# Kernel optimization log

Measured on AMD Instinct MI355X. Metric: run time of the kernel, lower is better.

The kernel has to match this reference:

```python
import jax, jax.numpy as jnp
import numpy as np

# Static configuration (matches init_kwargs)
B, D, H, W, C = 8, 4, 64, 64, 256
WS = (4, 8, 8)            # (temporal, h, w) window size
HEADS = 8
HD = C // HEADS
HID = 512                 # MLP hidden
N = WS[0] * WS[1] * WS[2]          # tokens per window = 256
INTERVAL = WS[1] * WS[2]           # tokens per frame in a window = 64
BW = B * (D // WS[0]) * (H // WS[1]) * (W // WS[2])  # total windows = 512
RPB_SIZE = (2 * WS[0] - 1) * (2 * WS[1] - 1) * (2 * WS[2] - 1)  # 1575


def _rel_index(ws):
    """Standard Swin-3D relative position index table, shape (N, N)."""
    d, h, w = ws
    coords = np.stack(np.meshgrid(np.arange(d), np.arange(h), np.arange(w), indexing='ij'))
    cf = coords.reshape(3, -1)
    rel = (cf[:, :, None] - cf[:, None, :]).transpose(1, 2, 0)
    rel[..., 0] += d - 1
    rel[..., 1] += h - 1
    rel[..., 2] += w - 1
    rel[..., 0] *= (2 * h - 1) * (2 * w - 1)
    rel[..., 1] *= (2 * w - 1)
    return rel.sum(-1)


_REL = _rel_index(WS)
# Per temporal group i: queries = frame i tokens, keys = all OTHER tokens (complement)
_KEY_IDS_NP = [np.array([j for j in range(N) if not (i * INTERVAL <= j < (i + 1) * INTERVAL)])
               for i in range(WS[0])]
KEY_IDS = [jnp.asarray(k) for k in _KEY_IDS_NP]
BIAS_IDX = [jnp.asarray(_REL[i * INTERVAL:(i + 1) * INTERVAL][:, _KEY_IDS_NP[i]])
            for i in range(WS[0])]


def setup_inputs() -> dict:
    key = jax.random.key(0)
    ks = jax.random.split(key, 8)
    s = jnp.float32(0.02)
    return {
        'x': jax.random.normal(ks[0], (B, D, H, W, C), jnp.float32),
        'ln1_g': jnp.ones((C,), jnp.float32), 'ln1_b': jnp.zeros((C,), jnp.float32),
        'ln2_g': jnp.ones((C,), jnp.float32), 'ln2_b': jnp.zeros((C,), jnp.float32),
        'wq': jax.random.normal(ks[1], (C, C), jnp.float32) * s,
        'wkv': jax.random.normal(ks[2], (C, 2 * C), jnp.float32) * s,
        'wp': jax.random.normal(ks[3], (C, C), jnp.float32) * s,
        'bp': jnp.zeros((C,), jnp.float32),
        'rpb': jax.random.normal(ks[4], (RPB_SIZE, HEADS), jnp.float32) * s,
        'w1': jax.random.normal(ks[5], (C, HID), jnp.float32) * s,
        'b1': jnp.zeros((HID,), jnp.float32),
        'w2': jax.random.normal(ks[6], (HID, C), jnp.float32) * s,
        'b2': jnp.zeros((C,), jnp.float32),
    }


def _ln(x, g, b):
    m = x.mean(-1, keepdims=True)
    v = ((x - m) ** 2).mean(-1, keepdims=True)
    return (x - m) * jax.lax.rsqrt(v + 1e-5) * g + b


def _partition(x):  # (B,D,H,W,C) -> (BW, N, C)
    x = x.reshape(B, D // WS[0], WS[0], H // WS[1], WS[1], W // WS[2], WS[2], C)
    return x.transpose(0, 1, 3, 5, 2, 4, 6, 7).reshape(BW, N, C)


def _reverse(xw):  # (BW, N, C) -> (B,D,H,W,C)
    x = xw.reshape(B, D // WS[0], H // WS[1], W // WS[2], WS[0], WS[1], WS[2], C)
    return x.transpose(0, 1, 4, 2, 5, 3, 6, 7).reshape(B, D, H, W, C)


def _window_attn(xw, wq, wkv, wp, bp, rpb):
    # q/k/v: (BW, heads, N, HD)
    q = (xw @ wq).reshape(BW, N, HEADS, HD).transpose(0, 2, 1, 3)
    kv = (xw @ wkv).reshape(BW, N, 2, HEADS, HD).transpose(2, 0, 3, 1, 4)
    k, v = kv[0], kv[1]
    scale = jnp.float32(HD ** -0.5)
    outs = []
    for i in range(WS[0]):  # loop over temporal groups (static, small)
        qs = q[:, :, i * INTERVAL:(i + 1) * INTERVAL] * scale   # (BW,h,Nq,HD)
        ks = k[:, :, KEY_IDS[i]]                                 # (BW,h,Nk,HD)
        vs = v[:, :, KEY_IDS[i]]
        bias = rpb[BIAS_IDX[i]].transpose(2, 0, 1)               # (h,Nq,Nk)
        a = jnp.einsum('bhqd,bhkd->bhqk', qs, ks) + bias[None]
        a = jax.nn.softmax(a, axis=-1)
        o = jnp.einsum('bhqk,bhkd->bhqd', a, vs)
        outs.append(o.transpose(0, 2, 1, 3).reshape(BW, INTERVAL, C))
    return jnp.concatenate(outs, axis=1) @ wp + bp


def reference(x, ln1_g, ln1_b, ln2_g, ln2_b, wq, wkv, wp, bp, rpb, w1, b1, w2, b2):
    xw = _partition(_ln(x, ln1_g, ln1_b))
    x = x + _reverse(_window_attn(xw, wq, wkv, wp, bp, rpb))
    h = jax.nn.gelu(_ln(x, ln2_g, ln2_b) @ w1 + b1, approximate=False)
    return x + h @ w2 + b2
```

## Files before the change

kernel.cpp:

```cpp
#include <hip/hip_runtime.h>

typedef unsigned short u16;
typedef __bf16 bf16x8 __attribute__((ext_vector_type(8)));
typedef float floatx4 __attribute__((ext_vector_type(4)));
typedef unsigned short u16x8 __attribute__((ext_vector_type(8)));

#define C_  256
#define NTOK 131072
#define QSCALE 0.17677669529663687f
#define RPB_N 1575

#define R1_ELEMS 33554432ull

__device__ u16 g_wT[524288];

__device__ __forceinline__ float bf2f(u16 u) {
    return __uint_as_float(((unsigned)u) << 16);
}
__device__ __forceinline__ u16 f2bf(float f) {
    unsigned u = __float_as_uint(f);
    return (u16)((u + 0x7FFFu + ((u >> 16) & 1u)) >> 16);
}

#define GL16(gsrc, ldst) __builtin_amdgcn_global_load_lds(                    \
    (const __attribute__((address_space(1))) void*)(gsrc),                    \
    (__attribute__((address_space(3))) void*)(ldst), 16, 0, 0)

__global__ __launch_bounds__(256) void wcvt_kernel(
    const float* __restrict__ W, int N, int ks, int ofs)
{
    const int idx = blockIdx.x * 256 + threadIdx.x;
    const int n = idx >> ks;
    const int k = idx & ((1 << ks) - 1);
    g_wT[ofs + idx] = f2bf(W[(size_t)k * N + n]);
}

__global__ __launch_bounds__(256) void ln_part_kernel(
    const float* __restrict__ x, const float* __restrict__ g, const float* __restrict__ bb,
    u16* __restrict__ xw)
{
    const int lane = threadIdx.x & 63;
    const int wave = threadIdx.x >> 6;
    const int t = blockIdx.x * 4 + wave;
    const int wb = t >> 8, n = t & 255;
    const int bidx = wb >> 6, hb = (wb >> 3) & 7, wbl = wb & 7;
    const int d = n >> 6, hh = (n >> 3) & 7, ww = n & 7;
    const size_t src = ((((size_t)bidx * 4 + d) * 64 + hb * 8 + hh) * 64 + wbl * 8 + ww) * C_;
    const int c0 = lane * 4;
    float4 raw = *reinterpret_cast<const float4*>(&x[src + c0]);
    float v0 = raw.x, v1 = raw.y, v2 = raw.z, v3 = raw.w;
    float s = v0 + v1 + v2 + v3;
    float sq = v0 * v0 + v1 * v1 + v2 * v2 + v3 * v3;
#pragma unroll
    for (int off = 32; off > 0; off >>= 1) {
        s  += __shfl_xor(s, off, 64);
        sq += __shfl_xor(sq, off, 64);
    }
    const float mean = s * (1.0f / 256.0f);
    const float var  = sq * (1.0f / 256.0f) - mean * mean;
    const float rstd = rsqrtf(var + 1e-5f);
    float4 gr = *reinterpret_cast<const float4*>(&g[c0]);
    float4 br = *reinterpret_cast<const float4*>(&bb[c0]);
    ushort4 outv;
    outv.x = f2bf((v0 - mean) * rstd * gr.x + br.x);
    outv.y = f2bf((v1 - mean) * rstd * gr.y + br.y);
    outv.z = f2bf((v2 - mean) * rstd * gr.z + br.z);
    outv.w = f2bf((v3 - mean) * rstd * gr.w + br.w);
    *reinterpret_cast<ushort4*>(&xw[(size_t)t * C_ + c0]) = outv;
}

__global__ __launch_bounds__(256) void resid_ln2_kernel(
    const float* __restrict__ x, const u16* __restrict__ oproj,
    const float* __restrict__ g, const float* __restrict__ bb,
    float* __restrict__ y, u16* __restrict__ xn)
{
    const int lane = threadIdx.x & 63;
    const int wave = threadIdx.x >> 6;
    const int t = blockIdx.x * 4 + wave;
    const int wpos = t & 63;
    const int h = (t >> 6) & 63;
    const int d = (t >> 12) & 3;
    const int bidx = t >> 14;
    const int wr = (((bidx * 8) + (h >> 3)) * 8 + (wpos >> 3)) * 256
                 + d * 64 + (h & 7) * 8 + (wpos & 7);
    const int c0 = lane * 4;
    float4 xr = *reinterpret_cast<const float4*>(&x[(size_t)t * C_ + c0]);
    ushort4 pr = *reinterpret_cast<const ushort4*>(&oproj[(size_t)wr * C_ + c0]);
    float v0 = xr.x + bf2f(pr.x);
    float v1 = xr.y + bf2f(pr.y);
    float v2 = xr.z + bf2f(pr.z);
    float v3 = xr.w + bf2f(pr.w);
    float s = v0 + v1 + v2 + v3;
    float sq = v0 * v0 + v1 * v1 + v2 * v2 + v3 * v3;
#pragma unroll
    for (int off = 32; off > 0; off >>= 1) {
        s  += __shfl_xor(s, off, 64);
        sq += __shfl_xor(sq, off, 64);
    }
    const float mean = s * (1.0f / 256.0f);
    const float var  = sq * (1.0f / 256.0f) - mean * mean;
    const float rstd = rsqrtf(var + 1e-5f);
    float4 yv; yv.x = v0; yv.y = v1; yv.z = v2; yv.w = v3;
    *reinterpret_cast<float4*>(&y[(size_t)t * C_ + c0]) = yv;
    float4 gr = *reinterpret_cast<const float4*>(&g[c0]);
    float4 br = *reinterpret_cast<const float4*>(&bb[c0]);
    ushort4 nv;
    nv.x = f2bf((v0 - mean) * rstd * gr.x + br.x);
    nv.y = f2bf((v1 - mean) * rstd * gr.y + br.y);
    nv.z = f2bf((v2 - mean) * rstd * gr.z + br.z);
    nv.w = f2bf((v3 - mean) * rstd * gr.w + br.w);
    *reinterpret_cast<ushort4*>(&xn[(size_t)t * C_ + c0]) = nv;
}

__global__ __launch_bounds__(256, 3) void gemm_v3_kernel(
    const u16* __restrict__ A, const u16* __restrict__ A2,
    int bofs, int kdim,
    u16* __restrict__ Cm, float* __restrict__ Cf, const float* __restrict__ bias,
    int mode)
{
    __shared__ __align__(16) u16 lds[2 * 10240];
    const int tid  = threadIdx.x;
    const int lane = tid & 63, wave = tid >> 6;
    const int lr = lane & 15, lq = lane >> 4;
    const int row0 = blockIdx.x * 64;
    const u16* Bt = &g_wT[bofs];

    const int s_row = lane >> 2;
    const int s_kel = (lane & 3) * 8;

    floatx4 acc[4][4] = {};
    const int NK = kdim >> 5;
    int cur = 0;

    auto STAGE = [&](int buf, int ks) {
        const int k0 = ks << 5;
        const u16* Asrc = A;
        int ka = k0;
        if (k0 >= 256) { Asrc = A2; ka = k0 - 256; }
        u16* lb = &lds[buf * 10240];
        GL16(&Asrc[(size_t)(row0 + wave * 16 + s_row) * 256 + ka + s_kel],
             lb + wave * 512 + lane * 8);
#pragma unroll
        for (int c = 0; c < 4; ++c) {
            const int s = wave * 4 + c;
            GL16(&Bt[(size_t)(s * 16 + s_row) * kdim + k0 + s_kel],
                 lb + 2048 + s * 512 + lane * 8);
        }
    };

    STAGE(0, 0);
    __syncthreads();

    for (int ks = 0; ks < NK; ++ks) {
        if (ks + 1 < NK) STAGE(cur ^ 1, ks + 1);
        const u16* lb = &lds[cur * 10240];
        bf16x8 af[4], bfv[4];
#pragma unroll
        for (int mt = 0; mt < 4; ++mt)
            af[mt] = *reinterpret_cast<const bf16x8*>(lb + (mt * 16 + lr) * 32 + lq * 8);
#pragma unroll
        for (int nt = 0; nt < 4; ++nt)
            bfv[nt] = *reinterpret_cast<const bf16x8*>(
                lb + 2048 + (wave * 64 + nt * 16 + lr) * 32 + lq * 8);
#pragma unroll
        for (int mt = 0; mt < 4; ++mt)
#pragma unroll
            for (int nt = 0; nt < 4; ++nt)
                acc[mt][nt] = __builtin_amdgcn_mfma_f32_16x16x32_bf16(
                    af[mt], bfv[nt], acc[mt][nt], 0, 0, 0);
        __syncthreads();
        cur ^= 1;
    }

    float* tw = reinterpret_cast<float*>(&lds[0]) + wave * (16 * 68);
#pragma unroll
    for (int mt = 0; mt < 4; ++mt) {
        asm volatile("s_waitcnt lgkmcnt(0)" ::: "memory");
        __builtin_amdgcn_sched_barrier(0);
#pragma unroll
        for (int nt = 0; nt < 4; ++nt) {
            const int col = wave * 64 + nt * 16 + lr;
            const float bs = (mode != 0) ? bias[col] : 0.0f;
#pragma unroll
            for (int r = 0; r < 4; ++r) {
                float v = acc[mt][nt][r] + bs;
                if (mode == 2) v = 0.5f * v * (1.0f + erff(v * 0.70710678118654752f));
                tw[(lq * 4 + r) * 68 + nt * 16 + lr] = v;
            }
        }
        asm volatile("s_waitcnt lgkmcnt(0)" ::: "memory");
        __builtin_amdgcn_sched_barrier(0);
        const int rrow = lane >> 2, grp = lane & 3;
        const float* src = &tw[rrow * 68 + grp * 16];
        float4 f0 = *reinterpret_cast<const float4*>(src + 0);
        float4 f1 = *reinterpret_cast<const float4*>(src + 4);
        float4 f2 = *reinterpret_cast<const float4*>(src + 8);
        float4 f3 = *reinterpret_cast<const float4*>(src + 12);
        const size_t gofs = (size_t)(row0 + mt * 16 + rrow) * 256 + wave * 64 + grp * 16;
        if (mode == 5) {
            float4* cp = reinterpret_cast<float4*>(&Cf[gofs]);
            float4 c0 = cp[0], c1 = cp[1], c2 = cp[2], c3 = cp[3];
            c0.x += f0.x; c0.y += f0.y; c0.z += f0.z; c0.w += f0.w;
            c1.x += f1.x; c1.y += f1.y; c1.z += f1.z; c1.w += f1.w;
            c2.x += f2.x; c2.y += f2.y; c2.z += f2.z; c2.w += f2.w;
            c3.x += f3.x; c3.y += f3.y; c3.z += f3.z; c3.w += f3.w;
            cp[0] = c0; cp[1] = c1; cp[2] = c2; cp[3] = c3;
        } else {
            const float tf[16] = {f0.x, f0.y, f0.z, f0.w, f1.x, f1.y, f1.z, f1.w,
                                  f2.x, f2.y, f2.z, f2.w, f3.x, f3.y, f3.z, f3.w};
            u16x8 o0, o1;
#pragma unroll
            for (int j = 0; j < 8; ++j) { o0[j] = f2bf(tf[j]); o1[j] = f2bf(tf[j + 8]); }
            *reinterpret_cast<u16x8*>(&Cm[gofs])     = o0;
            *reinterpret_cast<u16x8*>(&Cm[gofs + 8]) = o1;
        }
    }
}

__global__ __launch_bounds__(256) void attn_kernel(
    u16* __restrict__ qo, const u16* __restrict__ kb, const u16* __restrict__ vb,
    const float* __restrict__ rpbp)
{
    __shared__ __align__(16) u16 qh[64][40];
    __shared__ __align__(16) u16 kt[192][40];
    __shared__ __align__(16) u16 vtt[32][200];
    __shared__ __align__(16) u16 sp[64][200];
    __shared__ float biasld[RPB_N + 1];

    const int wb = blockIdx.x >> 2;
    const int i  = blockIdx.x & 3;
    const int tid = threadIdx.x;
    const int lane = tid & 63, wave = tid >> 6;
    const int lr = lane & 15, lq = lane >> 4;
    const size_t qbase = ((size_t)(wb * 256 + i * 64)) * C_;

    int relb[12][4];
    {
        const int q0 = wave * 16 + lq * 4;
#pragma unroll
        for (int r = 0; r < 4; ++r) {
            const int q = q0 + r;
            const int hq = q >> 3, wq_ = q & 7;
#pragma unroll
            for (int t = 0; t < 12; ++t) {
                const int kl = t * 16 + lr;
                const int nk = (kl < i * 64) ? kl : kl + 64;
                const int dk = nk >> 6, hk = (nk >> 3) & 7, wk = nk & 7;
                relb[t][r] = (i - dk + 3) * 225 + (hq - hk + 7) * 15 + (wq_ - wk + 7);
            }
        }
    }

    for (int h = 0; h < 8; ++h) {
        {
            const int row = tid >> 2, g = tid & 3;
            *reinterpret_cast<float4*>(&qh[row][g * 8]) =
                *reinterpret_cast<const float4*>(&qo[qbase + (size_t)row * C_ + h * 32 + g * 8]);
        }
#pragma unroll
        for (int t = 0; t < 3; ++t) {
            const int c = tid + t * 256;
            const int kl = c >> 2, g = c & 3;
            const int nk = (kl < i * 64) ? kl : kl + 64;
            const size_t base = ((size_t)(wb * 256 + nk)) * C_ + h * 32 + g * 8;
            *reinterpret_cast<float4*>(&kt[kl][g * 8]) =
                *reinterpret_cast<const float4*>(&kb[base]);
            u16x8 vv = *reinterpret_cast<const u16x8*>(&vb[base]);
#pragma unroll
            for (int j = 0; j < 8; ++j) vtt[g * 8 + j][kl] = vv[j];
        }
        for (int j = tid; j < RPB_N; j += 256) biasld[j] = rpbp[j * 8 + h];
        __syncthreads();

        floatx4 acc[12];
#pragma unroll
        for (int t = 0; t < 12; ++t) acc[t] = (floatx4){0.f, 0.f, 0.f, 0.f};
        {
            const bf16x8 af = *reinterpret_cast<const bf16x8*>(&qh[wave * 16 + lr][lq * 8]);
#pragma unroll
            for (int t = 0; t < 12; ++t) {
                const bf16x8 bfv = *reinterpret_cast<const bf16x8*>(&kt[t * 16 + lr][lq * 8]);
                acc[t] = __builtin_amdgcn_mfma_f32_16x16x32_bf16(af, bfv, acc[t], 0, 0, 0);
            }
        }

        float mrow[4] = {-1e30f, -1e30f, -1e30f, -1e30f};
#pragma unroll
        for (int t = 0; t < 12; ++t)
#pragma unroll
            for (int r = 0; r < 4; ++r) {
                const float v = fmaf(acc[t][r], QSCALE, biasld[relb[t][r]]);
                acc[t][r] = v;
                mrow[r] = fmaxf(mrow[r], v);
            }
#pragma unroll
        for (int off = 8; off >= 1; off >>= 1)
#pragma unroll
            for (int r = 0; r < 4; ++r)
                mrow[r] = fmaxf(mrow[r], __shfl_xor(mrow[r], off, 64));

        float srow[4] = {0.f, 0.f, 0.f, 0.f};
#pragma unroll
        for (int t = 0; t < 12; ++t)
#pragma unroll
            for (int r = 0; r < 4; ++r) {
                const float e = __expf(acc[t][r] - mrow[r]);
                acc[t][r] = e;
                srow[r] += e;
            }
#pragma unroll
        for (int off = 8; off >= 1; off >>= 1)
#pragma unroll
            for (int r = 0; r < 4; ++r)
                srow[r] += __shfl_xor(srow[r], off, 64);
#pragma unroll
        for (int r = 0; r < 4; ++r) srow[r] = 1.0f / srow[r];

#pragma unroll
        for (int t = 0; t < 12; ++t)
#pragma unroll
            for (int r = 0; r < 4; ++r)
                sp[wave * 16 + lq * 4 + r][t * 16 + lr] = f2bf(acc[t][r] * srow[r]);
        __syncthreads();

        floatx4 oacc[2];
        oacc[0] = (floatx4){0.f, 0.f, 0.f, 0.f};
        oacc[1] = (floatx4){0.f, 0.f, 0.f, 0.f};
#pragma unroll
        for (int kc = 0; kc < 6; ++kc) {
            const bf16x8 pa = *reinterpret_cast<const bf16x8*>(&sp[wave * 16 + lr][kc * 32 + lq * 8]);
#pragma unroll
            for (int nt = 0; nt < 2; ++nt) {
                const bf16x8 bv = *reinterpret_cast<const bf16x8*>(&vtt[nt * 16 + lr][kc * 32 + lq * 8]);
                oacc[nt] = __builtin_amdgcn_mfma_f32_16x16x32_bf16(pa, bv, oacc[nt], 0, 0, 0);
            }
        }
#pragma unroll
        for (int nt = 0; nt < 2; ++nt)
#pragma unroll
            for (int r = 0; r < 4; ++r)
                qo[qbase + (size_t)(wave * 16 + lq * 4 + r) * C_ + h * 32 + nt * 16 + lr] =
                    f2bf(oacc[nt][r]);
        __syncthreads();
    }
}

extern "C" void kernel_launch(void* const* d_in, const int* in_sizes, int n_in,
                              void* d_out, int out_size, void* d_ws, size_t ws_size,
                              hipStream_t stream) {
    const float* x    = (const float*)d_in[0];
    const float* ln1g = (const float*)d_in[1];
    const float* ln1b = (const float*)d_in[2];
    const float* ln2g = (const float*)d_in[3];
    const float* ln2b = (const float*)d_in[4];
    const float* wq   = (const float*)d_in[5];
    const float* wkv  = (const float*)d_in[6];
    const float* wp   = (const float*)d_in[7];
    const float* bp   = (const float*)d_in[8];
    const float* rpb  = (const float*)d_in[9];
    const float* w1   = (const float*)d_in[10];
    const float* b1   = (const float*)d_in[11];
    const float* w2   = (const float*)d_in[12];
    const float* b2   = (const float*)d_in[13];
    float* outf = (float*)d_out;
    u16*   outu = (u16*)d_out;
    u16*   ws16 = (u16*)d_ws;

    u16* r0 = ws16;
    u16* r1 = ws16 + R1_ELEMS;
    u16* kbuf = outu;
    u16* vbuf = outu + R1_ELEMS;

    wcvt_kernel<<<256, 256, 0, stream>>>(wq,  256, 8, 0);
    wcvt_kernel<<<512, 256, 0, stream>>>(wkv, 512, 8, 65536);
    wcvt_kernel<<<256, 256, 0, stream>>>(wp,  256, 8, 196608);
    wcvt_kernel<<<512, 256, 0, stream>>>(w1,  512, 8, 262144);
    wcvt_kernel<<<512, 256, 0, stream>>>(w2,  256, 9, 393216);

    ln_part_kernel<<<NTOK / 4, 256, 0, stream>>>(x, ln1g, ln1b, r0);

    gemm_v3_kernel<<<NTOK / 64, 256, 0, stream>>>(r0, r0, 65536,  256, kbuf, nullptr, nullptr, 0);
    gemm_v3_kernel<<<NTOK / 64, 256, 0, stream>>>(r0, r0, 131072, 256, vbuf, nullptr, nullptr, 0);
    gemm_v3_kernel<<<NTOK / 64, 256, 0, stream>>>(r0, r0, 0, 256, r0, nullptr, nullptr, 0);

    attn_kernel<<<512 * 4, 256, 0, stream>>>(r0, kbuf, vbuf, rpb);

    gemm_v3_kernel<<<NTOK / 64, 256, 0, stream>>>(r0, r0, 196608, 256, r0, nullptr, bp, 1);

    resid_ln2_kernel<<<NTOK / 4, 256, 0, stream>>>(x, r0, ln2g, ln2b, outf, r1);

    gemm_v3_kernel<<<NTOK / 64, 256, 0, stream>>>(r1, r1, 262144, 256, r0, nullptr, b1,       2);
    gemm_v3_kernel<<<NTOK / 64, 256, 0, stream>>>(r1, r1, 327680, 256, r1, nullptr, b1 + 256, 2);
    gemm_v3_kernel<<<NTOK / 64, 256, 0, stream>>>(r0, r1, 393216, 512, nullptr, outf, b2,     5);
}
```

Baseline: 961.1 us.

## Restructure attention: transposed V layout, precomputed bias table, direct global operand loads

The V projection GEMM now writes its output channel-major (transposed) so the attention kernel can read V fragments straight from global memory. A new kernel precomputes the relative position bias per (group, head, lane) in bf16, pre-scaled by log2e, so softmax can use exp2. The attention kernel drops its LDS staging of Q/K/V and bias and most of its barriers, loads MFMA operands directly from global, and remaps block indices so blocks sharing a window run close together for cache reuse. The cost is more uncoalesced global loads and bias rounded to bf16.

```diff
diff --git a/kernel.cpp b/kernel.cpp
--- a/kernel.cpp
+++ b/kernel.cpp
@@ -7,12 +7,13 @@
 
 #define C_  256
 #define NTOK 131072
-#define QSCALE 0.17677669529663687f
-#define RPB_N 1575
+#define QS2 0.25503488f
+#define LOG2E 1.4426950408889634f
 
 #define R1_ELEMS 33554432ull
 
 __device__ u16 g_wT[524288];
+__device__ u16 g_bexp[393216];
 
 __device__ __forceinline__ float bf2f(u16 u) {
     return __uint_as_float(((unsigned)u) << 16);
@@ -33,6 +34,27 @@
     const int n = idx >> ks;
     const int k = idx & ((1 << ks) - 1);
     g_wT[ofs + idx] = f2bf(W[(size_t)k * N + n]);
+}
+
+__global__ __launch_bounds__(256) void bexp_kernel(const float* __restrict__ rpb)
+{
+    const int i = blockIdx.x >> 3, h = blockIdx.x & 7;
+    const int tf = threadIdx.x;
+    const int w = tf >> 6, lq = (tf >> 4) & 3, lr = tf & 15;
+    u16* dst = &g_bexp[((size_t)(blockIdx.x * 256 + tf)) * 48];
+#pragma unroll
+    for (int t = 0; t < 12; ++t) {
+        const int kl = t * 16 + lr;
+        const int nk = (kl < i * 64) ? kl : kl + 64;
+        const int dk = nk >> 6, hk = (nk >> 3) & 7, wk = nk & 7;
+#pragma unroll
+        for (int r = 0; r < 4; ++r) {
+            const int q = w * 16 + lq * 4 + r;
+            const int hq = q >> 3, wq = q & 7;
+            const int rel = (i - dk + 3) * 225 + (hq - hk + 7) * 15 + (wq - wk + 7);
+            dst[t * 4 + r] = f2bf(rpb[rel * 8 + h] * LOG2E);
+        }
+    }
 }
 
 __global__ __launch_bounds__(256) void ln_part_kernel(
@@ -170,6 +192,23 @@
                     af[mt], bfv[nt], acc[mt][nt], 0, 0, 0);
         __syncthreads();
         cur ^= 1;
+    }
+
+    if (mode == 7) {
+#pragma unroll
+        for (int mt = 0; mt < 4; ++mt)
+#pragma unroll
+            for (int nt = 0; nt < 4; ++nt) {
+                const int col = wave * 64 + nt * 16 + lr;
+                const size_t tok = (size_t)row0 + mt * 16 + lq * 4;
+                ushort4 st;
+                st.x = f2bf(acc[mt][nt][0]);
+                st.y = f2bf(acc[mt][nt][1]);
+                st.z = f2bf(acc[mt][nt][2]);
+                st.w = f2bf(acc[mt][nt][3]);
+                *reinterpret_cast<ushort4*>(&Cm[(size_t)col * NTOK + tok]) = st;
+            }
+        return;
     }
 
     float* tw = reinterpret_cast<float*>(&lds[0]) + wave * (16 * 68);
@@ -217,79 +256,48 @@
     }
 }
 
-__global__ __launch_bounds__(256) void attn_kernel(
-    u16* __restrict__ qo, const u16* __restrict__ kb, const u16* __restrict__ vb,
-    const float* __restrict__ rpbp)
-{
-    __shared__ __align__(16) u16 qh[64][40];
-    __shared__ __align__(16) u16 kt[192][40];
-    __shared__ __align__(16) u16 vtt[32][200];
+__global__ __launch_bounds__(256, 3) void attn_kernel(
+    u16* __restrict__ qo, const u16* __restrict__ kb, const u16* __restrict__ vT)
+{
     __shared__ __align__(16) u16 sp[64][200];
-    __shared__ float biasld[RPB_N + 1];
-
-    const int wb = blockIdx.x >> 2;
-    const int i  = blockIdx.x & 3;
+
+    const int bid = blockIdx.x;
+    const int i  = (bid >> 3) & 3;
+    const int wb = (bid & 7) + (bid >> 5) * 8;
     const int tid = threadIdx.x;
     const int lane = tid & 63, wave = tid >> 6;
     const int lr = lane & 15, lq = lane >> 4;
     const size_t qbase = ((size_t)(wb * 256 + i * 64)) * C_;
-
-    int relb[12][4];
-    {
-        const int q0 = wave * 16 + lq * 4;
-#pragma unroll
-        for (int r = 0; r < 4; ++r) {
-            const int q = q0 + r;
-            const int hq = q >> 3, wq_ = q & 7;
-#pragma unroll
-            for (int t = 0; t < 12; ++t) {
-                const int kl = t * 16 + lr;
-                const int nk = (kl < i * 64) ? kl : kl + 64;
-                const int dk = nk >> 6, hk = (nk >> 3) & 7, wk = nk & 7;
-                relb[t][r] = (i - dk + 3) * 225 + (hq - hk + 7) * 15 + (wq_ - wk + 7);
-            }
-        }
-    }
+    const size_t kwin  = ((size_t)(wb * 256)) * C_;
+    const u16* bx = &g_bexp[((size_t)((i * 8) * 256) + (size_t)(wave * 64 + lq * 16 + lr)) * 48];
 
     for (int h = 0; h < 8; ++h) {
+        const int hc = h * 32;
+        u16x8 bvv[6];
         {
-            const int row = tid >> 2, g = tid & 3;
-            *reinterpret_cast<float4*>(&qh[row][g * 8]) =
-                *reinterpret_cast<const float4*>(&qo[qbase + (size_t)row * C_ + h * 32 + g * 8]);
-        }
-#pragma unroll
-        for (int t = 0; t < 3; ++t) {
-            const int c = tid + t * 256;
-            const int kl = c >> 2, g = c & 3;
-            const int nk = (kl < i * 64) ? kl : kl + 64;
-            const size_t base = ((size_t)(wb * 256 + nk)) * C_ + h * 32 + g * 8;
-            *reinterpret_cast<float4*>(&kt[kl][g * 8]) =
-                *reinterpret_cast<const float4*>(&kb[base]);
-            u16x8 vv = *reinterpret_cast<const u16x8*>(&vb[base]);
-#pragma unroll
-            for (int j = 0; j < 8; ++j) vtt[g * 8 + j][kl] = vv[j];
-        }
-        for (int j = tid; j < RPB_N; j += 256) biasld[j] = rpbp[j * 8 + h];
-        __syncthreads();
-
+            const u16* bl = bx + (size_t)h * 256 * 48;
+#pragma unroll
+            for (int v = 0; v < 6; ++v)
+                bvv[v] = *reinterpret_cast<const u16x8*>(bl + v * 8);
+        }
+        const bf16x8 af = *reinterpret_cast<const bf16x8*>(
+            &qo[qbase + (size_t)(wave * 16 + lr) * C_ + hc + lq * 8]);
         floatx4 acc[12];
 #pragma unroll
-        for (int t = 0; t < 12; ++t) acc[t] = (floatx4){0.f, 0.f, 0.f, 0.f};
-        {
-            const bf16x8 af = *reinterpret_cast<const bf16x8*>(&qh[wave * 16 + lr][lq * 8]);
-#pragma unroll
-            for (int t = 0; t < 12; ++t) {
-                const bf16x8 bfv = *reinterpret_cast<const bf16x8*>(&kt[t * 16 + lr][lq * 8]);
-                acc[t] = __builtin_amdgcn_mfma_f32_16x16x32_bf16(af, bfv, acc[t], 0, 0, 0);
-            }
-        }
-
+        for (int t = 0; t < 12; ++t) {
+            const int nrow = t * 16 + ((t * 16 >= i * 64) ? 64 : 0) + lr;
+            const bf16x8 bk = *reinterpret_cast<const bf16x8*>(
+                &kb[kwin + (size_t)nrow * C_ + hc + lq * 8]);
+            acc[t] = __builtin_amdgcn_mfma_f32_16x16x32_bf16(
+                af, bk, (floatx4){0.f, 0.f, 0.f, 0.f}, 0, 0, 0);
+        }
         float mrow[4] = {-1e30f, -1e30f, -1e30f, -1e30f};
 #pragma unroll
         for (int t = 0; t < 12; ++t)
 #pragma unroll
             for (int r = 0; r < 4; ++r) {
-                const float v = fmaf(acc[t][r], QSCALE, biasld[relb[t][r]]);
+                const int ii = t * 4 + r;
+                const float v = fmaf(acc[t][r], QS2, bf2f((u16)bvv[ii >> 3][ii & 7]));
                 acc[t][r] = v;
                 mrow[r] = fmaxf(mrow[r], v);
             }
@@ -298,13 +306,12 @@
 #pragma unroll
             for (int r = 0; r < 4; ++r)
                 mrow[r] = fmaxf(mrow[r], __shfl_xor(mrow[r], off, 64));
-
         float srow[4] = {0.f, 0.f, 0.f, 0.f};
 #pragma unroll
         for (int t = 0; t < 12; ++t)
 #pragma unroll
             for (int r = 0; r < 4; ++r) {
-                const float e = __expf(acc[t][r] - mrow[r]);
+                const float e = exp2f(acc[t][r] - mrow[r]);
                 acc[t][r] = e;
                 srow[r] += e;
             }
@@ -315,23 +322,24 @@
                 srow[r] += __shfl_xor(srow[r], off, 64);
 #pragma unroll
         for (int r = 0; r < 4; ++r) srow[r] = 1.0f / srow[r];
-
 #pragma unroll
         for (int t = 0; t < 12; ++t)
 #pragma unroll
             for (int r = 0; r < 4; ++r)
                 sp[wave * 16 + lq * 4 + r][t * 16 + lr] = f2bf(acc[t][r] * srow[r]);
-        __syncthreads();
-
         floatx4 oacc[2];
         oacc[0] = (floatx4){0.f, 0.f, 0.f, 0.f};
         oacc[1] = (floatx4){0.f, 0.f, 0.f, 0.f};
 #pragma unroll
         for (int kc = 0; kc < 6; ++kc) {
-            const bf16x8 pa = *reinterpret_cast<const bf16x8*>(&sp[wave * 16 + lr][kc * 32 + lq * 8]);
+            const bf16x8 pa = *reinterpret_cast<const bf16x8*>(
+                &sp[wave * 16 + lr][kc * 32 + lq * 8]);
+            const int kst = kc * 32 + lq * 8;
+            const int nk0 = kst + ((kst >= i * 64) ? 64 : 0);
 #pragma unroll
             for (int nt = 0; nt < 2; ++nt) {
-                const bf16x8 bv = *reinterpret_cast<const bf16x8*>(&vtt[nt * 16 + lr][kc * 32 + lq * 8]);
+                const bf16x8 bv = *reinterpret_cast<const bf16x8*>(
+                    &vT[(size_t)(hc + nt * 16 + lr) * NTOK + wb * 256 + nk0]);
                 oacc[nt] = __builtin_amdgcn_mfma_f32_16x16x32_bf16(pa, bv, oacc[nt], 0, 0, 0);
             }
         }
@@ -339,9 +347,8 @@
         for (int nt = 0; nt < 2; ++nt)
 #pragma unroll
             for (int r = 0; r < 4; ++r)
-                qo[qbase + (size_t)(wave * 16 + lq * 4 + r) * C_ + h * 32 + nt * 16 + lr] =
+                qo[qbase + (size_t)(wave * 16 + lq * 4 + r) * C_ + hc + nt * 16 + lr] =
                     f2bf(oacc[nt][r]);
-        __syncthreads();
     }
 }
 
@@ -369,21 +376,22 @@
     u16* r0 = ws16;
     u16* r1 = ws16 + R1_ELEMS;
     u16* kbuf = outu;
-    u16* vbuf = outu + R1_ELEMS;
+    u16* vTb  = outu + R1_ELEMS;
 
     wcvt_kernel<<<256, 256, 0, stream>>>(wq,  256, 8, 0);
     wcvt_kernel<<<512, 256, 0, stream>>>(wkv, 512, 8, 65536);
     wcvt_kernel<<<256, 256, 0, stream>>>(wp,  256, 8, 196608);
     wcvt_kernel<<<512, 256, 0, stream>>>(w1,  512, 8, 262144);
     wcvt_kernel<<<512, 256, 0, stream>>>(w2,  256, 9, 393216);
+    bexp_kernel<<<32, 256, 0, stream>>>(rpb);
 
     ln_part_kernel<<<NTOK / 4, 256, 0, stream>>>(x, ln1g, ln1b, r0);
 
     gemm_v3_kernel<<<NTOK / 64, 256, 0, stream>>>(r0, r0, 65536,  256, kbuf, nullptr, nullptr, 0);
-    gemm_v3_kernel<<<NTOK / 64, 256, 0, stream>>>(r0, r0, 131072, 256, vbuf, nullptr, nullptr, 0);
+    gemm_v3_kernel<<<NTOK / 64, 256, 0, stream>>>(r0, r0, 131072, 256, vTb,  nullptr, nullptr, 7);
     gemm_v3_kernel<<<NTOK / 64, 256, 0, stream>>>(r0, r0, 0, 256, r0, nullptr, nullptr, 0);
 
-    attn_kernel<<<512 * 4, 256, 0, stream>>>(r0, kbuf, vbuf, rpb);
+    attn_kernel<<<2048, 256, 0, stream>>>(r0, kbuf, vTb);
 
     gemm_v3_kernel<<<NTOK / 64, 256, 0, stream>>>(r0, r0, 196608, 256, r0, nullptr, bp, 1);
 
```

Measured after the change: 924.3 us. -3.8%, faster.
